# Optimization experiments

Measured on AMD Instinct MI355X. Metric: run time of the kernel, lower is better.

Reference implementation:

```python
import jax, jax.numpy as jnp
import numpy as np
import math

N_HEAD = 16
N_EMBD = 1024
HEAD_DIM = N_EMBD // N_HEAD
B, T = 2, 2048


def setup_inputs() -> dict:
    key = jax.random.key(0)
    k1, k2, k3 = jax.random.split(key, 3)
    scale = 0.02
    x = jax.random.normal(k1, (B, T, N_EMBD), dtype=jnp.float32)
    W_attn = jax.random.normal(k2, (N_EMBD, 3 * N_EMBD), dtype=jnp.float32) * scale
    b_attn = jnp.zeros((3 * N_EMBD,), dtype=jnp.float32)
    W_proj = jax.random.normal(k3, (N_EMBD, N_EMBD), dtype=jnp.float32) * scale
    b_proj = jnp.zeros((N_EMBD,), dtype=jnp.float32)
    return {"x": x, "W_attn": W_attn, "b_attn": b_attn, "W_proj": W_proj, "b_proj": b_proj}


def reference(x, W_attn, b_attn, W_proj, b_proj):
    b, t, c = x.shape
    qkv = x @ W_attn + b_attn                      # [B,T,3C]
    q, k, v = jnp.split(qkv, 3, axis=-1)
    # [B,T,C] -> [B,H,T,D]
    def heads(z):
        return z.reshape(b, t, N_HEAD, HEAD_DIM).transpose(0, 2, 1, 3)
    q, k, v = heads(q), heads(k), heads(v)
    att = jnp.einsum('bhqd,bhkd->bhqk', q, k) * (1.0 / math.sqrt(HEAD_DIM))
    causal = jnp.tril(jnp.ones((t, t), dtype=bool))  # [T,T]
    att = jnp.where(causal[None, None], att, -jnp.inf)
    att = jax.nn.softmax(att, axis=-1)
    y = jnp.einsum('bhqk,bhkd->bhqd', att, v)      # [B,H,T,D]
    y = y.transpose(0, 2, 1, 3).reshape(b, t, c)   # [B,T,C]
    return y @ W_proj + b_proj
```

## Files before the change

kernel.cpp:

```cpp
#include <hip/hip_runtime.h>
#include <hip/hip_bf16.h>


typedef __bf16 bf16_t;
typedef __bf16 bf16x8 __attribute__((ext_vector_type(8)));
typedef float f32x4 __attribute__((ext_vector_type(4)));
typedef unsigned short ushort_t;

#define QSCALE 0.18033688011f

__device__ __forceinline__ void glds16(const bf16_t* g, ushort_t* l) {
  __builtin_amdgcn_global_load_lds(
      (const __attribute__((address_space(1))) unsigned int*)g,
      (__attribute__((address_space(3))) unsigned int*)l, 16, 0, 0);
}

__global__ __launch_bounds__(256) void prep_kernel(
    const float* __restrict__ x, const float* __restrict__ W_attn,
    const float* __restrict__ W_proj, ushort_t* __restrict__ Xb,
    ushort_t* __restrict__ WtA, ushort_t* __restrict__ WtP) {
  const int bid = blockIdx.x, tid = threadIdx.x;
  if (bid < 4096) {
    int i = bid * 256 + tid;
    float4 v = ((const float4*)x)[i];
    ushort4 o;
    o.x = __builtin_bit_cast(unsigned short, (bf16_t)v.x);
    o.y = __builtin_bit_cast(unsigned short, (bf16_t)v.y);
    o.z = __builtin_bit_cast(unsigned short, (bf16_t)v.z);
    o.w = __builtin_bit_cast(unsigned short, (bf16_t)v.w);
    ((ushort4*)Xb)[i] = o;
    return;
  }
  __shared__ ushort_t tile[32][33];
  const float* in;
  ushort_t* out;
  int C, bx, by;
  if (bid < 4096 + 3072) { int idx = bid - 4096; in = W_attn; out = WtA; C = 3072; bx = idx % 96; by = idx / 96; }
  else                   { int idx = bid - 7168; in = W_proj; out = WtP; C = 1024; bx = idx % 32; by = idx / 32; }
  const int tx = tid & 31, ty = tid >> 5;
  int cbase = bx * 32, rbase = by * 32;
#pragma unroll
  for (int i = ty; i < 32; i += 8)
    tile[i][tx] = __builtin_bit_cast(
        unsigned short, (bf16_t)in[(size_t)(rbase + i) * C + cbase + tx]);
  __syncthreads();
#pragma unroll
  for (int i = ty; i < 32; i += 8)
    out[(size_t)(cbase + i) * 1024 + rbase + tx] = tile[tx][i];
}

__device__ __forceinline__ void gemm128_mainloop(
    const bf16_t* __restrict__ A, const bf16_t* __restrict__ Bt, int K,
    int mtile, int ntile, ushort_t* As, ushort_t* Bs, f32x4 acc[4][4]) {
  const int tid  = threadIdx.x;
  const int lane = tid & 63, wave = tid >> 6;
  const int l15  = lane & 15, quad = lane >> 4;
  const int wrow = (wave >> 1) * 64, wcol = (wave & 1) * 64;
  const int lr = lane >> 2;
  const int lc = (((lane & 3) ^ ((lr >> 1) & 3)) * 8);
  const bf16_t* Ap = A + (size_t)(mtile + wave * 32 + lr) * K + lc;
  const bf16_t* Bp = Bt + (size_t)(ntile + wave * 32 + lr) * K + lc;
  const int rsw = (quad ^ ((l15 >> 1) & 3)) * 8;
  const int woff = wave * 32 * 32;
#pragma unroll
  for (int c = 0; c < 2; c++) {
    glds16(Ap + (size_t)(c * 16) * K, As + woff + c * 16 * 32);
    glds16(Bp + (size_t)(c * 16) * K, Bs + woff + c * 16 * 32);
  }
  __syncthreads();
  const int nkb = K >> 5;
  for (int t = 0; t < nkb; t++) {
    const int cur = t & 1, nxt = cur ^ 1;
    if (t + 1 < nkb) {
#pragma unroll
      for (int c = 0; c < 2; c++) {
        glds16(Ap + (size_t)(c * 16) * K + (t + 1) * 32, As + nxt * 4096 + woff + c * 16 * 32);
        glds16(Bp + (size_t)(c * 16) * K + (t + 1) * 32, Bs + nxt * 4096 + woff + c * 16 * 32);
      }
    }
    bf16x8 af[4], bfr[4];
#pragma unroll
    for (int i = 0; i < 4; i++)
      af[i] = *(const bf16x8*)&As[cur * 4096 + (wrow + i * 16 + l15) * 32 + rsw];
#pragma unroll
    for (int j = 0; j < 4; j++)
      bfr[j] = *(const bf16x8*)&Bs[cur * 4096 + (wcol + j * 16 + l15) * 32 + rsw];
#pragma unroll
    for (int i = 0; i < 4; i++)
#pragma unroll
      for (int j = 0; j < 4; j++)
        acc[i][j] = __builtin_amdgcn_mfma_f32_16x16x32_bf16(af[i], bfr[j], acc[i][j], 0, 0, 0);
    __syncthreads();
  }
}

__global__ __launch_bounds__(256) void qkv_gemm_kernel(
    const bf16_t* __restrict__ X, const bf16_t* __restrict__ WtA,
    const float* __restrict__ bias, bf16_t* __restrict__ Qd,
    bf16_t* __restrict__ Kd, bf16_t* __restrict__ Vtd) {
  __shared__ ushort_t As[2 * 128 * 32];
  __shared__ ushort_t Bs[2 * 128 * 32];
  const int mtile = blockIdx.x * 128, ntile = blockIdx.y * 128;
  f32x4 acc[4][4] = {};
  gemm128_mainloop(X, WtA, 1024, mtile, ntile, As, Bs, acc);
  const int tid = threadIdx.x, lane = tid & 63, wave = tid >> 6;
  const int l15 = lane & 15, quad = lane >> 4;
  const int wrow = (wave >> 1) * 64, wcol = (wave & 1) * 64;
  const int sec = ntile >> 10;
  const int b = mtile >> 11;
  if (sec == 2) {
#pragma unroll
    for (int j = 0; j < 4; j++) {
      int n = ntile + wcol + j * 16 + l15;
      float bv = bias[n];
      int cc = n & 1023, h = cc >> 6, d = cc & 63;
      size_t bh = (size_t)(b * 16 + h);
#pragma unroll
      for (int i = 0; i < 4; i++) {
        int tbase = (mtile & 2047) + wrow + i * 16 + quad * 4;
        ushort4 o4;
        o4.x = __builtin_bit_cast(unsigned short, (bf16_t)(acc[i][j][0] + bv));
        o4.y = __builtin_bit_cast(unsigned short, (bf16_t)(acc[i][j][1] + bv));
        o4.z = __builtin_bit_cast(unsigned short, (bf16_t)(acc[i][j][2] + bv));
        o4.w = __builtin_bit_cast(unsigned short, (bf16_t)(acc[i][j][3] + bv));
        *(ushort4*)&Vtd[(bh * 64 + d) * 2048 + tbase] = o4;
      }
    }
    return;
  }
  const float sv = (sec == 0) ? QSCALE : 1.0f;
  bf16_t* Od = (sec == 0) ? Qd : Kd;
#pragma unroll
  for (int j = 0; j < 4; j++) {
    int n = ntile + wcol + j * 16 + l15;
    float bv = bias[n];
    int cc = n & 1023, h = cc >> 6, d = cc & 63;
    size_t bh = (size_t)(b * 16 + h);
#pragma unroll
    for (int i = 0; i < 4; i++) {
#pragma unroll
      for (int r = 0; r < 4; r++) {
        int t = (mtile & 2047) + wrow + i * 16 + quad * 4 + r;
        Od[(bh * 2048 + t) * 64 + d] = (bf16_t)((acc[i][j][r] + bv) * sv);
      }
    }
  }
}

__global__ __launch_bounds__(512) void attn_kernel(
    const bf16_t* __restrict__ Q, const bf16_t* __restrict__ K,
    const bf16_t* __restrict__ Vt, bf16_t* __restrict__ Y) {
  __shared__ ushort_t Ks[2][4096];
  __shared__ ushort_t Vs[2][4096];
  __shared__ ushort_t Ps[8][16 * 40];
  const int bh = blockIdx.y;
  const int qt = (blockIdx.y < 16) ? (15 - (int)blockIdx.x) : (int)blockIdx.x;
  const int tid = threadIdx.x, wave = tid >> 6, lane = tid & 63;
  const int l15 = lane & 15, quad = lane >> 4;
  const bf16_t* Qh = Q + (size_t)bh * 2048 * 64;
  const bf16_t* Kh = K + (size_t)bh * 2048 * 64;
  const bf16_t* Vh = Vt + (size_t)bh * 64 * 2048;
  const int b = bh >> 4, h = bh & 15;
  const int qw = qt * 128 + wave * 16;
  const int nkt = 2 * qt + 2;

  bf16x8 qa[2];
#pragma unroll
  for (int kc = 0; kc < 2; kc++)
    qa[kc] = *(const bf16x8*)(Qh + (size_t)(qw + l15) * 64 + kc * 32 + quad * 8);

  f32x4 o[4] = {};
  float lpart[4] = {};
  const int rsw = (quad ^ ((l15 >> 1) & 3)) * 8;

  const int lr4 = lane >> 2;
  const int csw = ((lane & 3) ^ ((lr4 >> 1) & 3)) * 8;
  const bool isK = wave < 4;
  const int sw = isK ? wave : wave - 4;
  const int rbase = (sw & 1) * 32;
  const bf16_t* gp0;
  size_t rowstep;
  if (isK) { gp0 = Kh + (size_t)(rbase + lr4) * 64 + (sw >> 1) * 32 + csw;  rowstep = 64; }
  else     { gp0 = Vh + (size_t)(rbase + lr4) * 2048 + (sw >> 1) * 32 + csw; rowstep = 2048; }
  const size_t kstep = isK ? (size_t)64 * 64 : 64;
  ushort_t* dst0 = (isK ? Ks[0] : Vs[0]) + (sw >> 1) * 2048 + rbase * 32;
  ushort_t* dst1 = (isK ? Ks[1] : Vs[1]) + (sw >> 1) * 2048 + rbase * 32;

#pragma unroll
  for (int c = 0; c < 2; c++)
    glds16(gp0 + (size_t)(c * 16) * rowstep, dst0 + c * 512);

  f32x4 zz = {0.f, 0.f, 0.f, 0.f};
  for (int kt = 0; kt < nkt; kt++) {
    const int cur = kt & 1;
    __syncthreads();
    if (kt + 1 < nkt) {
      ushort_t* nd = cur ? dst0 : dst1;
#pragma unroll
      for (int c = 0; c < 2; c++)
        glds16(gp0 + (size_t)(kt + 1) * kstep + (size_t)(c * 16) * rowstep, nd + c * 512);
    }
#pragma unroll
    for (int h32 = 0; h32 < 2; h32++) {
      const int kb32 = kt * 64 + h32 * 32;
      if (kb32 > qw + 15) break;
      bf16x8 kb[2][2];
#pragma unroll
      for (int bn = 0; bn < 2; bn++)
#pragma unroll
        for (int kc = 0; kc < 2; kc++)
          kb[bn][kc] = *(const bf16x8*)&Ks[cur][kc * 2048 + (h32 * 32 + bn * 16 + l15) * 32 + rsw];
      f32x4 s[2];
#pragma unroll
      for (int bn = 0; bn < 2; bn++) {
        f32x4 t0 = __builtin_amdgcn_mfma_f32_16x16x32_bf16(qa[0], kb[bn][0], zz, 0, 0, 0);
        s[bn] = __builtin_amdgcn_mfma_f32_16x16x32_bf16(qa[1], kb[bn][1], t0, 0, 0, 0);
      }
      const bool dg = (kb32 + 31 > qw);
#pragma unroll
      for (int r = 0; r < 4; r++) {
        int row = qw + quad * 4 + r;
        float v0 = s[0][r];
        float v1 = s[1][r];
        if (dg) {
          int c0 = kb32 + l15;
          if (c0 > row) v0 = -1e5f;
          if (c0 + 16 > row) v1 = -1e5f;
        }
        float p0 = __builtin_amdgcn_exp2f(v0);
        float p1 = __builtin_amdgcn_exp2f(v1);
        lpart[r] += p0 + p1;
        int prow = (quad * 4 + r) * 40;
        Ps[wave][prow + l15]      = __builtin_bit_cast(unsigned short, (bf16_t)p0);
        Ps[wave][prow + 16 + l15] = __builtin_bit_cast(unsigned short, (bf16_t)p1);
      }
      bf16x8 vb[4];
#pragma unroll
      for (int ns = 0; ns < 4; ns++)
        vb[ns] = *(const bf16x8*)&Vs[cur][h32 * 2048 + (ns * 16 + l15) * 32 + rsw];
      __asm__ volatile("" ::: "memory");
      bf16x8 pa = *(const bf16x8*)&Ps[wave][l15 * 40 + quad * 8];
#pragma unroll
      for (int ns = 0; ns < 4; ns++)
        o[ns] = __builtin_amdgcn_mfma_f32_16x16x32_bf16(pa, vb[ns], o[ns], 0, 0, 0);
    }
  }
#pragma unroll
  for (int r = 0; r < 4; r++) {
    float l = lpart[r];
#pragma unroll
    for (int off = 1; off < 16; off <<= 1) l += __shfl_xor(l, off);
    float inv_l = 1.0f / fmaxf(l, 1e-30f);
    int t = qw + quad * 4 + r;
#pragma unroll
    for (int ns = 0; ns < 4; ns++) {
      int c = h * 64 + ns * 16 + l15;
      Y[((size_t)(b * 2048 + t)) * 1024 + c] = (bf16_t)(o[ns][r] * inv_l);
    }
  }
}

__global__ __launch_bounds__(256) void proj_gemm_kernel(
    const bf16_t* __restrict__ Yb, const bf16_t* __restrict__ WtP,
    const float* __restrict__ bias, float* __restrict__ out) {
  __shared__ ushort_t As[2 * 128 * 32];
  __shared__ ushort_t Bs[2 * 64 * 32];
  const int tid = threadIdx.x;
  const int lane = tid & 63, wave = tid >> 6;
  const int l15 = lane & 15, quad = lane >> 4;
  const int wrow = (wave >> 1) * 64, wcol = (wave & 1) * 32;
  const int mtile = blockIdx.x * 128, ntile = blockIdx.y * 64;
  const int K = 1024;
  const int lr = lane >> 2;
  const int lc = (((lane & 3) ^ ((lr >> 1) & 3)) * 8);
  const bf16_t* Ap = Yb + (size_t)(mtile + wave * 32 + lr) * K + lc;
  const bf16_t* Bp = WtP + (size_t)(ntile + wave * 16 + lr) * K + lc;
  const int rsw = (quad ^ ((l15 >> 1) & 3)) * 8;
  const int wa = wave * 32 * 32, wb = wave * 16 * 32;
  f32x4 acc[4][2] = {};
  glds16(Ap, As + wa);
  glds16(Ap + (size_t)16 * K, As + wa + 16 * 32);
  glds16(Bp, Bs + wb);
  __syncthreads();
  for (int t = 0; t < 32; t++) {
    const int cur = t & 1, nxt = cur ^ 1;
    if (t + 1 < 32) {
      glds16(Ap + (t + 1) * 32, As + nxt * 4096 + wa);
      glds16(Ap + (size_t)16 * K + (t + 1) * 32, As + nxt * 4096 + wa + 16 * 32);
      glds16(Bp + (t + 1) * 32, Bs + nxt * 2048 + wb);
    }
    bf16x8 af[4], bfr[2];
#pragma unroll
    for (int i = 0; i < 4; i++)
      af[i] = *(const bf16x8*)&As[cur * 4096 + (wrow + i * 16 + l15) * 32 + rsw];
#pragma unroll
    for (int j = 0; j < 2; j++)
      bfr[j] = *(const bf16x8*)&Bs[cur * 2048 + (wcol + j * 16 + l15) * 32 + rsw];
#pragma unroll
    for (int i = 0; i < 4; i++)
#pragma unroll
      for (int j = 0; j < 2; j++)
        acc[i][j] = __builtin_amdgcn_mfma_f32_16x16x32_bf16(af[i], bfr[j], acc[i][j], 0, 0, 0);
    __syncthreads();
  }
#pragma unroll
  for (int j = 0; j < 2; j++) {
    int n = ntile + wcol + j * 16 + l15;
    float bv = bias[n];
#pragma unroll
    for (int i = 0; i < 4; i++) {
#pragma unroll
      for (int r = 0; r < 4; r++) {
        int m = mtile + wrow + i * 16 + quad * 4 + r;
        out[(size_t)m * 1024 + n] = acc[i][j][r] + bv;
      }
    }
  }
}

extern "C" void kernel_launch(void* const* d_in, const int* in_sizes, int n_in,
                              void* d_out, int out_size, void* d_ws, size_t ws_size,
                              hipStream_t stream) {
  const float* x      = (const float*)d_in[0];
  const float* W_attn = (const float*)d_in[1];
  const float* b_attn = (const float*)d_in[2];
  const float* W_proj = (const float*)d_in[3];
  const float* b_proj = (const float*)d_in[4];
  float* out = (float*)d_out;

  bf16_t* ws  = (bf16_t*)d_ws;
  bf16_t* WtA = ws;
  bf16_t* WtP = WtA + (size_t)3072 * 1024;
  bf16_t* Xb  = WtP + (size_t)1024 * 1024;
  bf16_t* Qb  = Xb + (size_t)4194304;
  bf16_t* Kb  = Qb + (size_t)4194304;
  bf16_t* Vtb = Kb + (size_t)4194304;
  bf16_t* Yb  = Vtb + (size_t)4194304;

  prep_kernel<<<8192, 256, 0, stream>>>(x, W_attn, W_proj,
      (ushort_t*)Xb, (ushort_t*)WtA, (ushort_t*)WtP);
  qkv_gemm_kernel<<<dim3(32, 24), 256, 0, stream>>>(Xb, WtA, b_attn, Qb, Kb, Vtb);
  attn_kernel<<<dim3(16, 32), 512, 0, stream>>>(Qb, Kb, Vtb, Yb);
  proj_gemm_kernel<<<dim3(32, 16), 256, 0, stream>>>(Yb, WtP, b_proj, out);
}
```

Before: 194.5 us.

## Triple-buffer QKV GEMM with explicit waitcnt; single-buffer projection GEMM

The QKV GEMM mainloop moves from double to triple-buffered LDS staging. Loads are issued two k-blocks ahead, and explicit s_waitcnt vmcnt / s_barrier with sched barriers replace the per-iteration __syncthreads, so global-to-LDS loads overlap more with MFMA work. The projection GEMM goes the other way: it becomes single-buffered with two barriers per k-step, which cuts LDS use but serializes loads and compute. The QKV change adds LDS pressure and relies on hand-tuned vmcnt counts for correctness.

```diff
diff --git a/kernel.cpp b/kernel.cpp
--- a/kernel.cpp
+++ b/kernel.cpp
@@ -62,44 +62,54 @@
   const bf16_t* Bp = Bt + (size_t)(ntile + wave * 32 + lr) * K + lc;
   const int rsw = (quad ^ ((l15 >> 1) & 3)) * 8;
   const int woff = wave * 32 * 32;
-#pragma unroll
-  for (int c = 0; c < 2; c++) {
-    glds16(Ap + (size_t)(c * 16) * K, As + woff + c * 16 * 32);
-    glds16(Bp + (size_t)(c * 16) * K, Bs + woff + c * 16 * 32);
-  }
-  __syncthreads();
   const int nkb = K >> 5;
+
+#define STAGE_QKV(s)                                                        \
+  {                                                                         \
+    ushort_t* Ad = As + ((s) % 3) * 4096 + woff;                            \
+    ushort_t* Bd = Bs + ((s) % 3) * 4096 + woff;                            \
+    _Pragma("unroll")                                                       \
+    for (int c = 0; c < 2; c++) {                                           \
+      glds16(Ap + (size_t)(c * 16) * K + (s) * 32, Ad + c * 512);           \
+      glds16(Bp + (size_t)(c * 16) * K + (s) * 32, Bd + c * 512);           \
+    }                                                                       \
+  }
+
+  STAGE_QKV(0);
+  STAGE_QKV(1);
   for (int t = 0; t < nkb; t++) {
-    const int cur = t & 1, nxt = cur ^ 1;
-    if (t + 1 < nkb) {
-#pragma unroll
-      for (int c = 0; c < 2; c++) {
-        glds16(Ap + (size_t)(c * 16) * K + (t + 1) * 32, As + nxt * 4096 + woff + c * 16 * 32);
-        glds16(Bp + (size_t)(c * 16) * K + (t + 1) * 32, Bs + nxt * 4096 + woff + c * 16 * 32);
-      }
-    }
+    if (t + 1 < nkb) asm volatile("s_waitcnt vmcnt(4)" ::: "memory");
+    else             asm volatile("s_waitcnt vmcnt(0)" ::: "memory");
+    __builtin_amdgcn_sched_barrier(0);
+    __builtin_amdgcn_s_barrier();
+    __builtin_amdgcn_sched_barrier(0);
+    if (t + 2 < nkb) STAGE_QKV(t + 2);
+    const int cur = (t % 3) * 4096;
     bf16x8 af[4], bfr[4];
 #pragma unroll
     for (int i = 0; i < 4; i++)
-      af[i] = *(const bf16x8*)&As[cur * 4096 + (wrow + i * 16 + l15) * 32 + rsw];
+      af[i] = *(const bf16x8*)&As[cur + (wrow + i * 16 + l15) * 32 + rsw];
 #pragma unroll
     for (int j = 0; j < 4; j++)
-      bfr[j] = *(const bf16x8*)&Bs[cur * 4096 + (wcol + j * 16 + l15) * 32 + rsw];
+      bfr[j] = *(const bf16x8*)&Bs[cur + (wcol + j * 16 + l15) * 32 + rsw];
 #pragma unroll
     for (int i = 0; i < 4; i++)
 #pragma unroll
       for (int j = 0; j < 4; j++)
         acc[i][j] = __builtin_amdgcn_mfma_f32_16x16x32_bf16(af[i], bfr[j], acc[i][j], 0, 0, 0);
-    __syncthreads();
-  }
+    __builtin_amdgcn_sched_barrier(0);
+    asm volatile("s_waitcnt lgkmcnt(0)" ::: "memory");
+    __builtin_amdgcn_sched_barrier(0);
+  }
+#undef STAGE_QKV
 }
 
 __global__ __launch_bounds__(256) void qkv_gemm_kernel(
     const bf16_t* __restrict__ X, const bf16_t* __restrict__ WtA,
     const float* __restrict__ bias, bf16_t* __restrict__ Qd,
     bf16_t* __restrict__ Kd, bf16_t* __restrict__ Vtd) {
-  __shared__ ushort_t As[2 * 128 * 32];
-  __shared__ ushort_t Bs[2 * 128 * 32];
+  __shared__ ushort_t As[3 * 128 * 32];
+  __shared__ ushort_t Bs[3 * 128 * 32];
   const int mtile = blockIdx.x * 128, ntile = blockIdx.y * 128;
   f32x4 acc[4][4] = {};
   gemm128_mainloop(X, WtA, 1024, mtile, ntile, As, Bs, acc);
@@ -263,8 +273,8 @@
 __global__ __launch_bounds__(256) void proj_gemm_kernel(
     const bf16_t* __restrict__ Yb, const bf16_t* __restrict__ WtP,
     const float* __restrict__ bias, float* __restrict__ out) {
-  __shared__ ushort_t As[2 * 128 * 32];
-  __shared__ ushort_t Bs[2 * 64 * 32];
+  __shared__ ushort_t As[128 * 32];
+  __shared__ ushort_t Bs[64 * 32];
   const int tid = threadIdx.x;
   const int lane = tid & 63, wave = tid >> 6;
   const int l15 = lane & 15, quad = lane >> 4;
@@ -276,32 +286,27 @@
   const bf16_t* Ap = Yb + (size_t)(mtile + wave * 32 + lr) * K + lc;
   const bf16_t* Bp = WtP + (size_t)(ntile + wave * 16 + lr) * K + lc;
   const int rsw = (quad ^ ((l15 >> 1) & 3)) * 8;
-  const int wa = wave * 32 * 32, wb = wave * 16 * 32;
+  ushort_t* Asw = As + wave * 32 * 32;
+  ushort_t* Bsw = Bs + wave * 16 * 32;
   f32x4 acc[4][2] = {};
-  glds16(Ap, As + wa);
-  glds16(Ap + (size_t)16 * K, As + wa + 16 * 32);
-  glds16(Bp, Bs + wb);
-  __syncthreads();
-  for (int t = 0; t < 32; t++) {
-    const int cur = t & 1, nxt = cur ^ 1;
-    if (t + 1 < 32) {
-      glds16(Ap + (t + 1) * 32, As + nxt * 4096 + wa);
-      glds16(Ap + (size_t)16 * K + (t + 1) * 32, As + nxt * 4096 + wa + 16 * 32);
-      glds16(Bp + (t + 1) * 32, Bs + nxt * 2048 + wb);
-    }
+  for (int kb = 0; kb < K; kb += 32) {
+    __syncthreads();
+    glds16(Ap + kb, Asw);
+    glds16(Ap + (size_t)16 * K + kb, Asw + 16 * 32);
+    glds16(Bp + kb, Bsw);
+    __syncthreads();
     bf16x8 af[4], bfr[2];
 #pragma unroll
     for (int i = 0; i < 4; i++)
-      af[i] = *(const bf16x8*)&As[cur * 4096 + (wrow + i * 16 + l15) * 32 + rsw];
+      af[i] = *(const bf16x8*)&As[(wrow + i * 16 + l15) * 32 + rsw];
 #pragma unroll
     for (int j = 0; j < 2; j++)
-      bfr[j] = *(const bf16x8*)&Bs[cur * 2048 + (wcol + j * 16 + l15) * 32 + rsw];
+      bfr[j] = *(const bf16x8*)&Bs[(wcol + j * 16 + l15) * 32 + rsw];
 #pragma unroll
     for (int i = 0; i < 4; i++)
 #pragma unroll
       for (int j = 0; j < 2; j++)
         acc[i][j] = __builtin_amdgcn_mfma_f32_16x16x32_bf16(af[i], bfr[j], acc[i][j], 0, 0, 0);
-    __syncthreads();
   }
 #pragma unroll
   for (int j = 0; j < 2; j++) {
```

After: 203.9 us. +4.9%, slower.
